# Kernel optimization log

Measured on AMD Instinct MI355X. Metric: run time of the kernel, lower is better.

Reference implementation:

```python
import jax, jax.numpy as jnp
import numpy as np

B, N = 32, 2048
NUM_FEATURE, NUM_CLUSTER, D_MODEL = 512, 256, 1024
LN_EPS = 1e-5
NEG_SLOPE = 0.2


def setup_inputs() -> dict:
    key = jax.random.key(0)
    ks = jax.random.split(key, 8)
    s_feat = 1.0 / np.sqrt(NUM_FEATURE)
    s_city = 1.0 / np.sqrt(NUM_CLUSTER)
    return {
        "input": jax.random.normal(ks[0], (B, N, NUM_FEATURE), dtype=jnp.float32),
        "static": jax.random.normal(ks[1], (N, NUM_CLUSTER), dtype=jnp.float32),
        # torch.nn.Linear stores weight as [out, in]
        "W_feat": jax.random.uniform(ks[2], (D_MODEL, NUM_FEATURE), jnp.float32, -s_feat, s_feat),
        "b_feat": jax.random.uniform(ks[3], (D_MODEL,), jnp.float32, -s_feat, s_feat),
        "W_city": jax.random.uniform(ks[4], (D_MODEL, NUM_CLUSTER), jnp.float32, -s_city, s_city),
        "b_city": jax.random.uniform(ks[5], (D_MODEL,), jnp.float32, -s_city, s_city),
        "gamma": jnp.ones((D_MODEL,), dtype=jnp.float32),
        "beta": jnp.zeros((D_MODEL,), dtype=jnp.float32),
    }


def reference(input, static, W_feat, b_feat, W_city, b_city, gamma, beta):
    # x = leaky_relu(feat_embed(input), 0.2)  -> [B, N, d_model]
    x = jnp.einsum("bnf,df->bnd", input, W_feat) + b_feat
    x = jnp.where(x >= 0, x, NEG_SLOPE * x)
    # c = city_embed(static) -> [N, d_model]; diag_embed + matmul == elementwise gate
    c = jnp.einsum("nk,dk->nd", static, W_city) + b_city
    x = x * c[None, :, :]
    # LayerNorm over d_model (eps=1e-5, elementwise affine)
    mu = jnp.mean(x, axis=-1, keepdims=True)
    var = jnp.mean(jnp.square(x - mu), axis=-1, keepdims=True)
    x = (x - mu) * jax.lax.rsqrt(var + LN_EPS)
    return x * gamma + beta
```

## Files before the change

kernel.cpp:

```cpp
#include <hip/hip_runtime.h>
#include <hip/hip_bf16.h>


typedef __attribute__((ext_vector_type(8))) short short8;
typedef __attribute__((ext_vector_type(4))) float f32x4;

__device__ __forceinline__ unsigned short f2bf(float f) {
    unsigned int u = __float_as_uint(f);
    unsigned int r = (u + 0x7FFFu + ((u >> 16) & 1u)) >> 16;
    return (unsigned short)r;
}
__device__ __forceinline__ float b2f(unsigned short h) {
    return __uint_as_float(((unsigned int)h) << 16);
}

#define LDS_ASYNC16(g, l) __builtin_amdgcn_global_load_lds(                 \
    (const __attribute__((address_space(1))) void*)(g),                     \
    (__attribute__((address_space(3))) void*)(l), 16, 0, 0)

__global__ __launch_bounds__(256) void convw_kernel(
    const float* __restrict__ w, unsigned short* __restrict__ o)
{
    int i = (blockIdx.x * 256 + threadIdx.x) * 4;
    float4 v = *(const float4*)(w + i);
    uint2 p;
    p.x = (unsigned)f2bf(v.x) | ((unsigned)f2bf(v.y) << 16);
    p.y = (unsigned)f2bf(v.z) | ((unsigned)f2bf(v.w) << 16);
    *(uint2*)(o + i) = p;
}

__global__ __launch_bounds__(256) void city_kernel(
    const float* __restrict__ st,
    const float* __restrict__ Wc,
    const float* __restrict__ bc,
    unsigned short* __restrict__ cg)
{
    __shared__ float Ss[32][260];
    __shared__ float Ws[32][260];
    const int tid = threadIdx.x;
    const int n0 = blockIdx.x << 5;
    const int d0 = blockIdx.y << 5;
    #pragma unroll
    for (int i = 0; i < 8; ++i) {
        int idx = (i << 8) + tid;
        int r   = idx >> 6;
        int c4  = (idx & 63) << 2;
        *(float4*)&Ss[r][c4] = *(const float4*)(st + (size_t)(n0 + r) * 256 + c4);
        *(float4*)&Ws[r][c4] = *(const float4*)(Wc + (size_t)(d0 + r) * 256 + c4);
    }
    __syncthreads();
    const int ti = tid >> 4, tj = tid & 15;
    const int r0 = ti << 1, c0 = tj << 1;
    float a00 = 0.f, a01 = 0.f, a10 = 0.f, a11 = 0.f;
    #pragma unroll 4
    for (int k = 0; k < 256; k += 4) {
        float4 x0 = *(const float4*)&Ss[r0][k];
        float4 x1 = *(const float4*)&Ss[r0 + 1][k];
        float4 y0 = *(const float4*)&Ws[c0][k];
        float4 y1 = *(const float4*)&Ws[c0 + 1][k];
        a00 += x0.x*y0.x + x0.y*y0.y + x0.z*y0.z + x0.w*y0.w;
        a01 += x0.x*y1.x + x0.y*y1.y + x0.z*y1.z + x0.w*y1.w;
        a10 += x1.x*y0.x + x1.y*y0.y + x1.z*y0.z + x1.w*y0.w;
        a11 += x1.x*y1.x + x1.y*y1.y + x1.z*y1.z + x1.w*y1.w;
    }
    const float b0 = bc[d0 + c0], b1 = bc[d0 + c0 + 1];
    cg[(size_t)(n0 + r0    ) * 1024 + d0 + c0    ] = f2bf(a00 + b0);
    cg[(size_t)(n0 + r0    ) * 1024 + d0 + c0 + 1] = f2bf(a01 + b1);
    cg[(size_t)(n0 + r0 + 1) * 1024 + d0 + c0    ] = f2bf(a10 + b0);
    cg[(size_t)(n0 + r0 + 1) * 1024 + d0 + c0 + 1] = f2bf(a11 + b1);
}

__global__ __launch_bounds__(512, 4) void feat_kernel(
    const float* __restrict__ inp,
    const unsigned short* __restrict__ Wf,
    const float* __restrict__ b_feat,
    const unsigned short* __restrict__ cg,
    const float* __restrict__ gamma,
    const float* __restrict__ beta,
    float* __restrict__ out)
{
    __shared__ unsigned short Bs[1024 * 32];
    __shared__ unsigned short As[32 * 40];
    __shared__ float red1[8][32];
    __shared__ float red2[8][32];
    __shared__ float smu[32], srs[32];

    const int tid  = threadIdx.x;
    const int lane = tid & 63;
    const int w    = tid >> 6;
    const int m0   = blockIdx.x * 32;
    const int n0   = m0 & 2047;

    f32x4 acc[2][8];
    #pragma unroll
    for (int i = 0; i < 2; ++i)
        #pragma unroll
        for (int j = 0; j < 8; ++j) acc[i][j] = (f32x4)0.f;

    const int ar = tid >> 4;
    const int ak = (tid & 15) << 1;
    const float* aptr = inp + (size_t)(m0 + ar) * 512 + ak;

    const int bd = (w << 4) + (lane >> 2);
    const unsigned short* bptr = Wf + (size_t)bd * 512 + ((lane & 3) << 3);
    unsigned short* bls = Bs + (w << 9);

    const int cl = lane & 15;
    const int q  = lane >> 4;

    for (int kb = 0; kb < 16; ++kb) {
        const int k0 = kb << 5;
        #pragma unroll
        for (int i = 0; i < 8; ++i) {
            LDS_ASYNC16(bptr + ((size_t)i << 16) + k0, bls + (i << 12));
        }
        float2 af = *(const float2*)(aptr + k0);
        *(unsigned int*)(As + ar * 40 + ak) =
            (unsigned)f2bf(af.x) | ((unsigned)f2bf(af.y) << 16);
        __syncthreads();

        const unsigned short* arow = As + cl * 40 + (q << 3);
        short8 a0 = *(const short8*)(arow);
        short8 a1 = *(const short8*)(arow + 16 * 40);
        const unsigned short* bbase = Bs + (((w << 7) + cl) << 5) + (q << 3);
        #pragma unroll
        for (int ct = 0; ct < 8; ++ct) {
            short8 b = *(const short8*)(bbase + (ct << 9));
            acc[0][ct] = __builtin_amdgcn_mfma_f32_16x16x32_bf16(a0, b, acc[0][ct], 0, 0, 0);
            acc[1][ct] = __builtin_amdgcn_mfma_f32_16x16x32_bf16(a1, b, acc[1][ct], 0, 0, 0);
        }
        __syncthreads();
    }

    float s1[2][4], s2[2][4];
    #pragma unroll
    for (int rt = 0; rt < 2; ++rt)
        #pragma unroll
        for (int r = 0; r < 4; ++r) { s1[rt][r] = 0.f; s2[rt][r] = 0.f; }

    #pragma unroll
    for (int ct = 0; ct < 8; ++ct) {
        const int d = (w << 7) + (ct << 4) + cl;
        const float bf = b_feat[d];
        #pragma unroll
        for (int rt = 0; rt < 2; ++rt) {
            #pragma unroll
            for (int r = 0; r < 4; ++r) {
                const int row = (rt << 4) + (q << 2) + r;
                float x = acc[rt][ct][r] + bf;
                x = (x >= 0.f) ? x : 0.2f * x;
                x *= b2f(cg[(size_t)(n0 + row) * 1024 + d]);
                acc[rt][ct][r] = x;
                s1[rt][r] += x;
                s2[rt][r] += x * x;
            }
        }
    }
    #pragma unroll
    for (int off = 1; off < 16; off <<= 1) {
        #pragma unroll
        for (int rt = 0; rt < 2; ++rt)
            #pragma unroll
            for (int r = 0; r < 4; ++r) {
                s1[rt][r] += __shfl_xor(s1[rt][r], off, 64);
                s2[rt][r] += __shfl_xor(s2[rt][r], off, 64);
            }
    }
    if (cl == 0) {
        #pragma unroll
        for (int rt = 0; rt < 2; ++rt)
            #pragma unroll
            for (int r = 0; r < 4; ++r) {
                const int row = (rt << 4) + (q << 2) + r;
                red1[w][row] = s1[rt][r];
                red2[w][row] = s2[rt][r];
            }
    }
    __syncthreads();
    if (tid < 32) {
        float a = 0.f, b = 0.f;
        #pragma unroll
        for (int j = 0; j < 8; ++j) { a += red1[j][tid]; b += red2[j][tid]; }
        const float mu  = a * (1.0f / 1024.0f);
        const float var = b * (1.0f / 1024.0f) - mu * mu;
        smu[tid] = mu;
        srs[tid] = rsqrtf(var + 1e-5f);
    }
    __syncthreads();

    #pragma unroll
    for (int ct = 0; ct < 8; ++ct) {
        const int d = (w << 7) + (ct << 4) + cl;
        const float g = gamma[d], be = beta[d];
        #pragma unroll
        for (int rt = 0; rt < 2; ++rt) {
            #pragma unroll
            for (int r = 0; r < 4; ++r) {
                const int row = (rt << 4) + (q << 2) + r;
                out[(size_t)(m0 + row) * 1024 + d] =
                    (acc[rt][ct][r] - smu[row]) * srs[row] * g + be;
            }
        }
    }
}

extern "C" void kernel_launch(void* const* d_in, const int* in_sizes, int n_in,
                              void* d_out, int out_size, void* d_ws, size_t ws_size,
                              hipStream_t stream) {
    const float* inp   = (const float*)d_in[0];
    const float* st    = (const float*)d_in[1];
    const float* Wf    = (const float*)d_in[2];
    const float* bfeat = (const float*)d_in[3];
    const float* Wc    = (const float*)d_in[4];
    const float* bc    = (const float*)d_in[5];
    const float* gamma = (const float*)d_in[6];
    const float* beta  = (const float*)d_in[7];
    float* out = (float*)d_out;

    unsigned short* wsWf = (unsigned short*)d_ws;
    unsigned short* wsC  = (unsigned short*)((char*)d_ws + (1 << 20));

    convw_kernel<<<512, 256, 0, stream>>>(Wf, wsWf);
    city_kernel<<<dim3(64, 32), 256, 0, stream>>>(st, Wc, bc, wsC);
    feat_kernel<<<2048, 512, 0, stream>>>(inp, wsWf, bfeat, wsC, gamma, beta, out);
}
```

Baseline: 592.7 us.

## Double-buffer feat GEMM with 64-row tiles and use MFMA for city GEMM

The main kernel now processes 64 rows per block instead of 32, which halves how often the full bf16 weight is streamed from global memory into LDS. It double-buffers the weight and activation tiles, prefetching the next k-slice while MFMAs run on the current one, and drops one barrier per iteration. The city embedding kernel is rewritten to convert its operands to bf16 and use MFMA instructions instead of scalar fp32 FMAs. In exchange, LDS use doubles and register pressure rises, so only two blocks per CU are allowed, and the city gate is now computed from bf16-rounded inputs.

```diff
diff --git a/kernel.cpp b/kernel.cpp
--- a/kernel.cpp
+++ b/kernel.cpp
@@ -7,8 +7,7 @@
 
 __device__ __forceinline__ unsigned short f2bf(float f) {
     unsigned int u = __float_as_uint(f);
-    unsigned int r = (u + 0x7FFFu + ((u >> 16) & 1u)) >> 16;
-    return (unsigned short)r;
+    return (unsigned short)((u + 0x7FFFu + ((u >> 16) & 1u)) >> 16);
 }
 __device__ __forceinline__ float b2f(unsigned short h) {
     return __uint_as_float(((unsigned int)h) << 16);
@@ -35,42 +34,71 @@
     const float* __restrict__ bc,
     unsigned short* __restrict__ cg)
 {
-    __shared__ float Ss[32][260];
-    __shared__ float Ws[32][260];
-    const int tid = threadIdx.x;
-    const int n0 = blockIdx.x << 5;
-    const int d0 = blockIdx.y << 5;
-    #pragma unroll
-    for (int i = 0; i < 8; ++i) {
-        int idx = (i << 8) + tid;
-        int r   = idx >> 6;
-        int c4  = (idx & 63) << 2;
-        *(float4*)&Ss[r][c4] = *(const float4*)(st + (size_t)(n0 + r) * 256 + c4);
-        *(float4*)&Ws[r][c4] = *(const float4*)(Wc + (size_t)(d0 + r) * 256 + c4);
-    }
-    __syncthreads();
-    const int ti = tid >> 4, tj = tid & 15;
-    const int r0 = ti << 1, c0 = tj << 1;
-    float a00 = 0.f, a01 = 0.f, a10 = 0.f, a11 = 0.f;
-    #pragma unroll 4
-    for (int k = 0; k < 256; k += 4) {
-        float4 x0 = *(const float4*)&Ss[r0][k];
-        float4 x1 = *(const float4*)&Ss[r0 + 1][k];
-        float4 y0 = *(const float4*)&Ws[c0][k];
-        float4 y1 = *(const float4*)&Ws[c0 + 1][k];
-        a00 += x0.x*y0.x + x0.y*y0.y + x0.z*y0.z + x0.w*y0.w;
-        a01 += x0.x*y1.x + x0.y*y1.y + x0.z*y1.z + x0.w*y1.w;
-        a10 += x1.x*y0.x + x1.y*y0.y + x1.z*y0.z + x1.w*y0.w;
-        a11 += x1.x*y1.x + x1.y*y1.y + x1.z*y1.z + x1.w*y1.w;
-    }
-    const float b0 = bc[d0 + c0], b1 = bc[d0 + c0 + 1];
-    cg[(size_t)(n0 + r0    ) * 1024 + d0 + c0    ] = f2bf(a00 + b0);
-    cg[(size_t)(n0 + r0    ) * 1024 + d0 + c0 + 1] = f2bf(a01 + b1);
-    cg[(size_t)(n0 + r0 + 1) * 1024 + d0 + c0    ] = f2bf(a10 + b0);
-    cg[(size_t)(n0 + r0 + 1) * 1024 + d0 + c0 + 1] = f2bf(a11 + b1);
-}
-
-__global__ __launch_bounds__(512, 4) void feat_kernel(
+    __shared__ __align__(16) unsigned short Sa[64 * 264];
+    __shared__ __align__(16) unsigned short Sb[128 * 264];
+    const int t  = threadIdx.x;
+    const int n0 = blockIdx.x << 6;
+    const int d0 = blockIdx.y << 7;
+
+    #pragma unroll
+    for (int i = 0; i < 16; ++i) {
+        int idx = (i << 8) + t;
+        int row = idx >> 6, kq = (idx & 63) << 2;
+        float4 v = *(const float4*)(st + (size_t)(n0 + row) * 256 + kq);
+        uint2 p;
+        p.x = (unsigned)f2bf(v.x) | ((unsigned)f2bf(v.y) << 16);
+        p.y = (unsigned)f2bf(v.z) | ((unsigned)f2bf(v.w) << 16);
+        *(uint2*)(Sa + row * 264 + kq) = p;
+    }
+    #pragma unroll
+    for (int i = 0; i < 32; ++i) {
+        int idx = (i << 8) + t;
+        int row = idx >> 6, kq = (idx & 63) << 2;
+        float4 v = *(const float4*)(Wc + (size_t)(d0 + row) * 256 + kq);
+        uint2 p;
+        p.x = (unsigned)f2bf(v.x) | ((unsigned)f2bf(v.y) << 16);
+        p.y = (unsigned)f2bf(v.z) | ((unsigned)f2bf(v.w) << 16);
+        *(uint2*)(Sb + row * 264 + kq) = p;
+    }
+    __syncthreads();
+
+    const int wv = t >> 6;
+    const int cl = t & 15, q = (t >> 4) & 3;
+    f32x4 acc[4][2];
+    #pragma unroll
+    for (int rt = 0; rt < 4; ++rt)
+        #pragma unroll
+        for (int ct = 0; ct < 2; ++ct) acc[rt][ct] = (f32x4)0.f;
+
+    #pragma unroll
+    for (int ks = 0; ks < 8; ++ks) {
+        short8 a[4];
+        #pragma unroll
+        for (int rt = 0; rt < 4; ++rt)
+            a[rt] = *(const short8*)(Sa + ((rt << 4) + cl) * 264 + (ks << 5) + (q << 3));
+        #pragma unroll
+        for (int ct = 0; ct < 2; ++ct) {
+            short8 bf8 = *(const short8*)(Sb + ((wv << 5) + (ct << 4) + cl) * 264 + (ks << 5) + (q << 3));
+            #pragma unroll
+            for (int rt = 0; rt < 4; ++rt)
+                acc[rt][ct] = __builtin_amdgcn_mfma_f32_16x16x32_bf16(a[rt], bf8, acc[rt][ct], 0, 0, 0);
+        }
+    }
+    #pragma unroll
+    for (int ct = 0; ct < 2; ++ct) {
+        const int d = d0 + (wv << 5) + (ct << 4) + cl;
+        const float bcv = bc[d];
+        #pragma unroll
+        for (int rt = 0; rt < 4; ++rt)
+            #pragma unroll
+            for (int rr = 0; rr < 4; ++rr) {
+                const int row = (rt << 4) + (q << 2) + rr;
+                cg[(size_t)(n0 + row) * 1024 + d] = f2bf(acc[rt][ct][rr] + bcv);
+            }
+    }
+}
+
+__global__ __launch_bounds__(512, 2) void feat_kernel(
     const float* __restrict__ inp,
     const unsigned short* __restrict__ Wf,
     const float* __restrict__ b_feat,
@@ -79,112 +107,115 @@
     const float* __restrict__ beta,
     float* __restrict__ out)
 {
-    __shared__ unsigned short Bs[1024 * 32];
-    __shared__ unsigned short As[32 * 40];
-    __shared__ float red1[8][32];
-    __shared__ float red2[8][32];
-    __shared__ float smu[32], srs[32];
-
-    const int tid  = threadIdx.x;
-    const int lane = tid & 63;
-    const int w    = tid >> 6;
-    const int m0   = blockIdx.x * 32;
+    __shared__ __align__(16) unsigned short Bs[2][32768];
+    __shared__ __align__(16) unsigned short As[2][2560];
+
+    const int t    = threadIdx.x;
+    const int lane = t & 63;
+    const int w    = t >> 6;
+    const int cl   = lane & 15;
+    const int q    = lane >> 4;
+    const int m0   = blockIdx.x << 6;
     const int n0   = m0 & 2047;
 
-    f32x4 acc[2][8];
-    #pragma unroll
-    for (int i = 0; i < 2; ++i)
-        #pragma unroll
-        for (int j = 0; j < 8; ++j) acc[i][j] = (f32x4)0.f;
-
-    const int ar = tid >> 4;
-    const int ak = (tid & 15) << 1;
-    const float* aptr = inp + (size_t)(m0 + ar) * 512 + ak;
-
-    const int bd = (w << 4) + (lane >> 2);
-    const unsigned short* bptr = Wf + (size_t)bd * 512 + ((lane & 3) << 3);
-    unsigned short* bls = Bs + (w << 9);
-
-    const int cl = lane & 15;
-    const int q  = lane >> 4;
+    f32x4 acc[4][8];
+    #pragma unroll
+    for (int rt = 0; rt < 4; ++rt)
+        #pragma unroll
+        for (int ct = 0; ct < 8; ++ct) acc[rt][ct] = (f32x4)0.f;
+
+    const int arow = t >> 3, akq = (t & 7) << 2;
+    const float* ap = inp + (size_t)(m0 + arow) * 512 + akq;
+
+    const unsigned short* bgp = Wf + (size_t)((w << 4) + cl) * 512 + (q << 3);
+
+    #pragma unroll
+    for (int i = 0; i < 8; ++i)
+        LDS_ASYNC16(bgp + ((size_t)i << 16), &Bs[0][(w << 9) + (i << 12)]);
+    {
+        float4 av = *(const float4*)ap;
+        uint2 p;
+        p.x = (unsigned)f2bf(av.x) | ((unsigned)f2bf(av.y) << 16);
+        p.y = (unsigned)f2bf(av.z) | ((unsigned)f2bf(av.w) << 16);
+        *(uint2*)(&As[0][arow * 40 + akq]) = p;
+    }
+    __syncthreads();
 
     for (int kb = 0; kb < 16; ++kb) {
-        const int k0 = kb << 5;
-        #pragma unroll
-        for (int i = 0; i < 8; ++i) {
-            LDS_ASYNC16(bptr + ((size_t)i << 16) + k0, bls + (i << 12));
-        }
-        float2 af = *(const float2*)(aptr + k0);
-        *(unsigned int*)(As + ar * 40 + ak) =
-            (unsigned)f2bf(af.x) | ((unsigned)f2bf(af.y) << 16);
+        const int b = kb & 1;
+        float4 av;
+        if (kb < 15) {
+            const int k0n = (kb + 1) << 5;
+            #pragma unroll
+            for (int i = 0; i < 8; ++i)
+                LDS_ASYNC16(bgp + k0n + ((size_t)i << 16), &Bs[b ^ 1][(w << 9) + (i << 12)]);
+            av = *(const float4*)(ap + k0n);
+        }
+        short8 a[4];
+        #pragma unroll
+        for (int rt = 0; rt < 4; ++rt)
+            a[rt] = *(const short8*)(&As[b][((rt << 4) + cl) * 40 + (q << 3)]);
+        #pragma unroll
+        for (int ct = 0; ct < 8; ++ct) {
+            short8 bf8 = *(const short8*)(&Bs[b][(((w << 3) + ct) << 9) + (q << 7) + (cl << 3)]);
+            #pragma unroll
+            for (int rt = 0; rt < 4; ++rt)
+                acc[rt][ct] = __builtin_amdgcn_mfma_f32_16x16x32_bf16(a[rt], bf8, acc[rt][ct], 0, 0, 0);
+        }
+        if (kb < 15) {
+            uint2 p;
+            p.x = (unsigned)f2bf(av.x) | ((unsigned)f2bf(av.y) << 16);
+            p.y = (unsigned)f2bf(av.z) | ((unsigned)f2bf(av.w) << 16);
+            *(uint2*)(&As[b ^ 1][arow * 40 + akq]) = p;
+        }
         __syncthreads();
-
-        const unsigned short* arow = As + cl * 40 + (q << 3);
-        short8 a0 = *(const short8*)(arow);
-        short8 a1 = *(const short8*)(arow + 16 * 40);
-        const unsigned short* bbase = Bs + (((w << 7) + cl) << 5) + (q << 3);
-        #pragma unroll
-        for (int ct = 0; ct < 8; ++ct) {
-            short8 b = *(const short8*)(bbase + (ct << 9));
-            acc[0][ct] = __builtin_amdgcn_mfma_f32_16x16x32_bf16(a0, b, acc[0][ct], 0, 0, 0);
-            acc[1][ct] = __builtin_amdgcn_mfma_f32_16x16x32_bf16(a1, b, acc[1][ct], 0, 0, 0);
-        }
-        __syncthreads();
-    }
-
-    float s1[2][4], s2[2][4];
-    #pragma unroll
-    for (int rt = 0; rt < 2; ++rt)
-        #pragma unroll
-        for (int r = 0; r < 4; ++r) { s1[rt][r] = 0.f; s2[rt][r] = 0.f; }
-
-    #pragma unroll
-    for (int ct = 0; ct < 8; ++ct) {
-        const int d = (w << 7) + (ct << 4) + cl;
-        const float bf = b_feat[d];
-        #pragma unroll
-        for (int rt = 0; rt < 2; ++rt) {
-            #pragma unroll
-            for (int r = 0; r < 4; ++r) {
-                const int row = (rt << 4) + (q << 2) + r;
-                float x = acc[rt][ct][r] + bf;
+    }
+
+    float* red1 = (float*)&As[0][0];
+    float* red2 = red1 + 512;
+    float* smu  = red1 + 1024;
+    float* srs  = red1 + 1088;
+
+    float bfv[8];
+    #pragma unroll
+    for (int ct = 0; ct < 8; ++ct) bfv[ct] = b_feat[(w << 7) + (ct << 4) + cl];
+
+    #pragma unroll
+    for (int rt = 0; rt < 4; ++rt) {
+        #pragma unroll
+        for (int rr = 0; rr < 4; ++rr) {
+            const int row = (rt << 4) + (q << 2) + rr;
+            float s1 = 0.f, s2 = 0.f;
+            #pragma unroll
+            for (int ct = 0; ct < 8; ++ct) {
+                const int d = (w << 7) + (ct << 4) + cl;
+                float x = acc[rt][ct][rr] + bfv[ct];
                 x = (x >= 0.f) ? x : 0.2f * x;
                 x *= b2f(cg[(size_t)(n0 + row) * 1024 + d]);
-                acc[rt][ct][r] = x;
-                s1[rt][r] += x;
-                s2[rt][r] += x * x;
-            }
-        }
-    }
-    #pragma unroll
-    for (int off = 1; off < 16; off <<= 1) {
-        #pragma unroll
-        for (int rt = 0; rt < 2; ++rt)
-            #pragma unroll
-            for (int r = 0; r < 4; ++r) {
-                s1[rt][r] += __shfl_xor(s1[rt][r], off, 64);
-                s2[rt][r] += __shfl_xor(s2[rt][r], off, 64);
-            }
-    }
-    if (cl == 0) {
-        #pragma unroll
-        for (int rt = 0; rt < 2; ++rt)
-            #pragma unroll
-            for (int r = 0; r < 4; ++r) {
-                const int row = (rt << 4) + (q << 2) + r;
-                red1[w][row] = s1[rt][r];
-                red2[w][row] = s2[rt][r];
-            }
-    }
-    __syncthreads();
-    if (tid < 32) {
-        float a = 0.f, b = 0.f;
-        #pragma unroll
-        for (int j = 0; j < 8; ++j) { a += red1[j][tid]; b += red2[j][tid]; }
+                acc[rt][ct][rr] = x;
+                s1 += x;
+                s2 += x * x;
+            }
+            #pragma unroll
+            for (int off = 1; off < 16; off <<= 1) {
+                s1 += __shfl_xor(s1, off, 64);
+                s2 += __shfl_xor(s2, off, 64);
+            }
+            if (cl == 0) {
+                red1[(w << 6) + row] = s1;
+                red2[(w << 6) + row] = s2;
+            }
+        }
+    }
+    __syncthreads();
+    if (t < 64) {
+        float a = 0.f, bb = 0.f;
+        #pragma unroll
+        for (int j = 0; j < 8; ++j) { a += red1[(j << 6) + t]; bb += red2[(j << 6) + t]; }
         const float mu  = a * (1.0f / 1024.0f);
-        const float var = b * (1.0f / 1024.0f) - mu * mu;
-        smu[tid] = mu;
-        srs[tid] = rsqrtf(var + 1e-5f);
+        const float var = bb * (1.0f / 1024.0f) - mu * mu;
+        smu[t] = mu;
+        srs[t] = rsqrtf(var + 1e-5f);
     }
     __syncthreads();
 
@@ -193,12 +224,12 @@
         const int d = (w << 7) + (ct << 4) + cl;
         const float g = gamma[d], be = beta[d];
         #pragma unroll
-        for (int rt = 0; rt < 2; ++rt) {
-            #pragma unroll
-            for (int r = 0; r < 4; ++r) {
-                const int row = (rt << 4) + (q << 2) + r;
+        for (int rt = 0; rt < 4; ++rt) {
+            #pragma unroll
+            for (int rr = 0; rr < 4; ++rr) {
+                const int row = (rt << 4) + (q << 2) + rr;
                 out[(size_t)(m0 + row) * 1024 + d] =
-                    (acc[rt][ct][r] - smu[row]) * srs[row] * g + be;
+                    (acc[rt][ct][rr] - smu[row]) * srs[row] * g + be;
             }
         }
     }
@@ -221,6 +252,6 @@
     unsigned short* wsC  = (unsigned short*)((char*)d_ws + (1 << 20));
 
     convw_kernel<<<512, 256, 0, stream>>>(Wf, wsWf);
-    city_kernel<<<dim3(64, 32), 256, 0, stream>>>(st, Wc, bc, wsC);
-    feat_kernel<<<2048, 512, 0, stream>>>(inp, wsWf, bfeat, wsC, gamma, beta, out);
-}
+    city_kernel<<<dim3(32, 8), 256, 0, stream>>>(st, Wc, bc, wsC);
+    feat_kernel<<<1024, 512, 0, stream>>>(inp, wsWf, bfeat, wsC, gamma, beta, out);
+}
```

Measured after the change: 580.2 us. -2.1%, faster.
